# Kernel optimization log

Hardware: AMD Instinct MI355X
Metric: run time of the kernel (lower is better)

The kernel has to match this reference:

```python
import jax, jax.numpy as jnp
import numpy as np

N_NODES = 20000
DEG = 6
E = N_NODES * DEG  # 120000 edges == line-graph nodes
D_NODE, D_EDGE = 64, 16
HID, OUT = 128, 128
EPS = 1e-5


def setup_inputs() -> dict:
    key = jax.random.key(0)
    ks = jax.random.split(key, 8)
    rng = np.random.default_rng(0)
    # graph: each node is the source of DEG edges (direction='out' -> index_r = edge_index[0])
    src = np.repeat(np.arange(N_NODES), DEG)
    dst = rng.integers(0, N_NODES, E)
    edge_index = np.stack([src, dst]).astype(np.int64)
    # two_step_index: ordered pairs of distinct edges sharing a source node
    # (bipartite 2-hop, self loops removed), then GATConv add_self_loops re-appends (i,i)
    ii, jj = np.meshgrid(np.arange(DEG), np.arange(DEG), indexing='ij')
    off = ~np.eye(DEG, dtype=bool)
    ii, jj = ii[off], jj[off]  # DEG*(DEG-1) within-group pairs
    base = (np.arange(N_NODES) * DEG)[:, None]
    s2 = np.concatenate([(base + ii[None, :]).ravel(), np.arange(E)])
    d2 = np.concatenate([(base + jj[None, :]).ravel(), np.arange(E)])
    index_2step = np.stack([s2, d2]).astype(np.int64)  # [2, 720000]
    d_in = D_NODE + D_EDGE
    return {
        "edge_attr": jax.random.normal(ks[0], (E, D_EDGE), jnp.float32),
        "node_attr": jax.random.normal(ks[1], (N_NODES, D_NODE), jnp.float32),
        "bn0_g": jnp.ones((d_in,), jnp.float32),
        "bn0_b": jnp.zeros((d_in,), jnp.float32),
        "W1": jax.random.normal(ks[2], (d_in, HID), jnp.float32) / np.sqrt(d_in).astype(np.float32),
        "bn1_g": jnp.ones((HID,), jnp.float32),
        "bn1_b": jnp.zeros((HID,), jnp.float32),
        "Wg": jax.random.normal(ks[3], (HID, OUT), jnp.float32) / np.sqrt(HID).astype(np.float32),
        "att_src": jax.random.normal(ks[4], (OUT,), jnp.float32) * 0.1,
        "att_dst": jax.random.normal(ks[5], (OUT,), jnp.float32) * 0.1,
        "gat_bias": jnp.zeros((OUT,), jnp.float32),
        "bnf_g": jnp.ones((OUT,), jnp.float32),
        "bnf_b": jnp.zeros((OUT,), jnp.float32),
        "edge_index": jnp.asarray(edge_index),
        "index_2step": jnp.asarray(index_2step),
        "num_nodes": N_NODES,
    }


def batch_norm(x, g, b):
    # training-mode BatchNorm1d (biased variance), like the torch module default
    mu = x.mean(0)
    var = x.var(0)
    return (x - mu) * jax.lax.rsqrt(var + EPS) * g + b


def reference(edge_attr, node_attr, bn0_g, bn0_b, W1, bn1_g, bn1_b,
              Wg, att_src, att_dst, gat_bias, bnf_g, bnf_b,
              edge_index, index_2step, num_nodes):
    index_r = edge_index[0]  # [E] source node of each edge (direction='out')
    # h0: per-edge concat of source-node attrs and edge attrs  [E, Dn+De]
    h0 = jnp.concatenate([node_attr[index_r], edge_attr], axis=1)
    # linear encoder: BN -> Linear(no bias) -> BN -> ReLU (dropout p=0)
    h1 = jax.nn.relu(batch_norm(batch_norm(h0, bn0_g, bn0_b) @ W1, bn1_g, bn1_b))
    # --- GATConv (heads=1) on the line graph given by index_2step ---
    E_ = h1.shape[0]
    x = h1 @ Wg                 # [E, OUT]
    a_src = x @ att_src         # [E]
    a_dst = x @ att_dst         # [E]
    s, d = index_2step[0], index_2step[1]
    e = jax.nn.leaky_relu(a_src[s] + a_dst[d], 0.2)          # [E2]
    e = e - jax.ops.segment_max(e, d, num_segments=E_)[d]    # stable edge-softmax
    ex = jnp.exp(e)
    alpha = ex / (jax.ops.segment_sum(ex, d, num_segments=E_)[d] + 1e-16)
    h2 = jax.ops.segment_sum(alpha[:, None] * x[s], d, num_segments=E_) + gat_bias
    # --- global_add_pool keyed by source node id, then final BatchNorm ---
    h3 = jax.ops.segment_sum(h2, index_r, num_segments=num_nodes)  # [N, OUT]
    return batch_norm(h3, bnf_g, bnf_b)
```

## Files before the change

### kernel.cpp

```cpp
#include <hip/hip_runtime.h>

#define N_NODES 20000
#define DEG 6
#define E_EDGES 120000
#define EPS_BN 1e-5f
#define NBLK 2500
#define EB 48
#define NB 8

#define WS_S0SUM 0
#define WS_S0SQ  80
#define WS_BIAS1 160
#define WS_S1SUM 288
#define WS_S1SQ  1312
#define WS_SC1M  2336
#define WS_SH1M  2464
#define WS_FSUM  2592
#define WS_FSQ   2720
#define WS_STATS_FLOATS 2848
#define WS_WT1   2848
#define WS_WGT   8992

typedef float f32x4 __attribute__((ext_vector_type(4)));
typedef short bf16x8 __attribute__((ext_vector_type(8)));

__device__ __forceinline__ unsigned short f2bf(float f) {
  unsigned u = __float_as_uint(f);
  u += 0x7fffu + ((u >> 16) & 1u);
  return (unsigned short)(u >> 16);
}
__device__ __forceinline__ unsigned pack2bf(float a, float b) {
  return (unsigned)f2bf(a) | ((unsigned)f2bf(b) << 16);
}

__global__ __launch_bounds__(256) void k1_bn0_stats(
    const float* __restrict__ node_attr, const float* __restrict__ edge_attr,
    float* __restrict__ ws) {
  __shared__ float red[256];
  const int t = threadIdx.x;
  const int b = blockIdx.x;
  if (b < 128) {
    const int c = t & 63, rl = t >> 6;
    float s = 0.f, q = 0.f;
    for (int row = b * 4 + rl; row < N_NODES; row += 512) {
      float v = node_attr[row * 64 + c];
      s += v; q += v * v;
    }
    red[t] = s;
    __syncthreads();
    if (t < 64) atomicAdd(&ws[WS_S0SUM + t], red[t] + red[t + 64] + red[t + 128] + red[t + 192]);
    __syncthreads();
    red[t] = q;
    __syncthreads();
    if (t < 64) atomicAdd(&ws[WS_S0SQ + t], red[t] + red[t + 64] + red[t + 128] + red[t + 192]);
  } else {
    const int c = t & 15, rl = t >> 4;
    float s = 0.f, q = 0.f;
    for (int row = (b - 128) * 16 + rl; row < E_EDGES; row += 2048) {
      float v = edge_attr[row * 16 + c];
      s += v; q += v * v;
    }
    red[t] = s;
    __syncthreads();
    if (t < 16) {
      float tot = 0.f;
      #pragma unroll
      for (int k = 0; k < 16; ++k) tot += red[t + 16 * k];
      atomicAdd(&ws[WS_S0SUM + 64 + t], tot);
    }
    __syncthreads();
    red[t] = q;
    __syncthreads();
    if (t < 16) {
      float tot = 0.f;
      #pragma unroll
      for (int k = 0; k < 16; ++k) tot += red[t + 16 * k];
      atomicAdd(&ws[WS_S0SQ + 64 + t], tot);
    }
  }
}

__global__ __launch_bounds__(256) void k0_fold(
    const float* __restrict__ W1, const float* __restrict__ Wg,
    const float* __restrict__ bn0_g, const float* __restrict__ bn0_b,
    float* __restrict__ ws) {
  short* wt1 = (short*)(ws + WS_WT1);
  short* wgt = (short*)(ws + WS_WGT);
  const int t0 = blockIdx.x * 256 + threadIdx.x;
  for (int i = t0; i < 128 * 96; i += 32 * 256) {
    int n = i / 96, k = i % 96;
    float v = 0.f;
    if (k < 80) {
      float cnt = (k < 64) ? (float)N_NODES : (float)E_EDGES;
      float mu = ws[WS_S0SUM + k] / cnt;
      float var = ws[WS_S0SQ + k] / cnt - mu * mu;
      v = W1[k * 128 + n] * (bn0_g[k] * rsqrtf(var + EPS_BN));
    }
    wt1[i] = (short)f2bf(v);
  }
  for (int i = t0; i < 128 * 128; i += 32 * 256) {
    int n = i >> 7, k = i & 127;
    wgt[i] = (short)f2bf(Wg[k * 128 + n]);
  }
  if (blockIdx.x == 0 && threadIdx.x < 128) {
    int n = threadIdx.x;
    float s = 0.f;
    for (int k = 0; k < 80; ++k) {
      float cnt = (k < 64) ? (float)N_NODES : (float)E_EDGES;
      float mu = ws[WS_S0SUM + k] / cnt;
      float var = ws[WS_S0SQ + k] / cnt - mu * mu;
      float sc = bn0_g[k] * rsqrtf(var + EPS_BN);
      s += (bn0_b[k] - mu * sc) * W1[k * 128 + n];
    }
    ws[WS_BIAS1 + n] = s;
  }
}

#define STAGE_INPUTS()                                                         \
  if (t < NB * 16) {                                                           \
    int row = t >> 4, c4 = (t & 15) << 2;                                      \
    float4 v = *(const float4*)&node_attr[(size_t)(g * NB + row) * 64 + c4];   \
    *(uint2*)&n0s[row * 72 + c4] = make_uint2(pack2bf(v.x, v.y), pack2bf(v.z, v.w)); \
  }                                                                            \
  if (t < EB * 4) {                                                            \
    int row = t >> 2, c4 = (t & 3) << 2;                                       \
    float4 v = *(const float4*)&edge_attr[(size_t)(g * EB + row) * 16 + c4];   \
    *(uint2*)&e0s[row * 24 + c4] = make_uint2(pack2bf(v.x, v.y), pack2bf(v.z, v.w)); \
  }                                                                            \
  if (t < 8) zpad[t] = 0;

#define GEMM1_CORE(acc1)                                                       \
  _Pragma("unroll")                                                            \
  for (int ks = 0; ks < 3; ++ks) {                                             \
    bf16x8 bb0 = *(const bf16x8*)&wt1[(Nb + lm) * 96 + ks * 32 + lq * 8];      \
    bf16x8 bb1 = *(const bf16x8*)&wt1[(Nb + 16 + lm) * 96 + ks * 32 + lq * 8]; \
    _Pragma("unroll")                                                          \
    for (int mt = 0; mt < 3; ++mt) {                                           \
      const short* ap;                                                         \
      if (ks < 2) ap = &n0s[rowdiv6[mt] * 72 + ks * 32 + lq * 8];              \
      else ap = (lq < 2) ? &e0s[(mt * 16 + lm) * 24 + lq * 8] : zpad;          \
      bf16x8 a = *(const bf16x8*)ap;                                           \
      acc1[mt][0] = __builtin_amdgcn_mfma_f32_16x16x32_bf16(a, bb0, acc1[mt][0], 0, 0, 0); \
      acc1[mt][1] = __builtin_amdgcn_mfma_f32_16x16x32_bf16(a, bb1, acc1[mt][1], 0, 0, 0); \
    }                                                                          \
  }

__global__ __launch_bounds__(256, 6) void k2_bn1_stats(
    const float* __restrict__ node_attr, const float* __restrict__ edge_attr,
    float* __restrict__ ws) {
  __shared__ __align__(16) short n0s[NB * 72];
  __shared__ __align__(16) short e0s[EB * 24];
  __shared__ __align__(16) short zpad[8];
  const int t = threadIdx.x;
  const int g = blockIdx.x;
  const int l = t & 63, wid = t >> 6;
  const int lm = l & 15, lq = l >> 4;
  const int Nb = wid * 32;
  const short* wt1 = (const short*)(ws + WS_WT1);
  int rowdiv6[3];
  #pragma unroll
  for (int mt = 0; mt < 3; ++mt) rowdiv6[mt] = (mt * 16 + lm) / 6;
  float bias1c[2];
  bias1c[0] = ws[WS_BIAS1 + Nb + lm];
  bias1c[1] = ws[WS_BIAS1 + Nb + 16 + lm];
  STAGE_INPUTS();
  __syncthreads();
  f32x4 acc1[3][2] = {};
  GEMM1_CORE(acc1);
  const int set = g & 7;
  #pragma unroll
  for (int nt = 0; nt < 2; ++nt) {
    float s = 0.f, q = 0.f;
    #pragma unroll
    for (int mt = 0; mt < 3; ++mt)
      #pragma unroll
      for (int r = 0; r < 4; ++r) {
        float v = acc1[mt][nt][r] + bias1c[nt];
        s += v; q += v * v;
      }
    s += __shfl_xor(s, 16); s += __shfl_xor(s, 32);
    q += __shfl_xor(q, 16); q += __shfl_xor(q, 32);
    if (l < 16) {
      int col = Nb + nt * 16 + lm;
      atomicAdd(&ws[WS_S1SUM + set * 128 + col], s);
      atomicAdd(&ws[WS_S1SQ + set * 128 + col], q);
    }
  }
}

__global__ __launch_bounds__(128) void k2b_finalize(
    const float* __restrict__ bn1_g, const float* __restrict__ bn1_b,
    float* __restrict__ ws) {
  const int t = threadIdx.x;
  float s = 0.f, q = 0.f;
  #pragma unroll
  for (int st = 0; st < 8; ++st) {
    s += ws[WS_S1SUM + st * 128 + t];
    q += ws[WS_S1SQ + st * 128 + t];
  }
  const float invE = 1.f / (float)E_EDGES;
  float mu = s * invE;
  float var = q * invE - mu * mu;
  float sc1 = bn1_g[t] * rsqrtf(var + EPS_BN);
  float sh1 = bn1_b[t] - mu * sc1;
  ws[WS_SC1M + t] = sc1;
  ws[WS_SH1M + t] = ws[WS_BIAS1 + t] * sc1 + sh1;
}

__global__ __launch_bounds__(256, 6) void k3_fused(
    const float* __restrict__ node_attr, const float* __restrict__ edge_attr,
    const float* __restrict__ att_src, const float* __restrict__ att_dst,
    const float* __restrict__ gat_bias,
    float* __restrict__ out, float* __restrict__ ws) {
  __shared__ __align__(16) short n0s[NB * 72];
  __shared__ __align__(16) short e0s[EB * 24];
  __shared__ __align__(16) short zpad[8];
  __shared__ __align__(16) short h1s[EB * 136];
  __shared__ float asP[4][EB], adP[4][EB];
  __shared__ float asS[EB], adS[EB], wSm[EB];
  __shared__ float h3L[NB * 128];

  const int t = threadIdx.x;
  const int g = blockIdx.x;
  const int l = t & 63, wid = t >> 6;
  const int lm = l & 15, lq = l >> 4;
  const int Nb = wid * 32;
  const short* wt1 = (const short*)(ws + WS_WT1);
  const short* wgt = (const short*)(ws + WS_WGT);
  int rowdiv6[3];
  #pragma unroll
  for (int mt = 0; mt < 3; ++mt) rowdiv6[mt] = (mt * 16 + lm) / 6;
  float sc1c[2], sh1c[2], atS[2], atD[2];
  #pragma unroll
  for (int nt = 0; nt < 2; ++nt) {
    int col = Nb + nt * 16 + lm;
    sc1c[nt] = ws[WS_SC1M + col];
    sh1c[nt] = ws[WS_SH1M + col];
    atS[nt] = att_src[col];
    atD[nt] = att_dst[col];
  }
  *(f32x4*)&h3L[t * 4] = (f32x4){0.f, 0.f, 0.f, 0.f};
  STAGE_INPUTS();
  __syncthreads();
  {
    f32x4 acc1[3][2] = {};
    GEMM1_CORE(acc1);
    #pragma unroll
    for (int mt = 0; mt < 3; ++mt)
      #pragma unroll
      for (int nt = 0; nt < 2; ++nt)
        #pragma unroll
        for (int r = 0; r < 4; ++r) {
          int row = mt * 16 + lq * 4 + r;
          int col = Nb + nt * 16 + lm;
          float v = fmaxf(acc1[mt][nt][r] * sc1c[nt] + sh1c[nt], 0.f);
          h1s[row * 136 + col] = (short)f2bf(v);
        }
  }
  __syncthreads();
  f32x4 acc2[3][2] = {};
  #pragma unroll
  for (int ks = 0; ks < 4; ++ks) {
    bf16x8 bb0 = *(const bf16x8*)&wgt[(Nb + lm) * 128 + ks * 32 + lq * 8];
    bf16x8 bb1 = *(const bf16x8*)&wgt[(Nb + 16 + lm) * 128 + ks * 32 + lq * 8];
    #pragma unroll
    for (int mt = 0; mt < 3; ++mt) {
      bf16x8 a = *(const bf16x8*)&h1s[(mt * 16 + lm) * 136 + ks * 32 + lq * 8];
      acc2[mt][0] = __builtin_amdgcn_mfma_f32_16x16x32_bf16(a, bb0, acc2[mt][0], 0, 0, 0);
      acc2[mt][1] = __builtin_amdgcn_mfma_f32_16x16x32_bf16(a, bb1, acc2[mt][1], 0, 0, 0);
    }
  }
  #pragma unroll
  for (int mt = 0; mt < 3; ++mt)
    #pragma unroll
    for (int r = 0; r < 4; ++r) {
      float ps = acc2[mt][0][r] * atS[0] + acc2[mt][1][r] * atS[1];
      float pd = acc2[mt][0][r] * atD[0] + acc2[mt][1][r] * atD[1];
      #pragma unroll
      for (int off = 1; off < 16; off <<= 1) {
        ps += __shfl_xor(ps, off);
        pd += __shfl_xor(pd, off);
      }
      if (lm == 0) {
        int row = mt * 16 + lq * 4 + r;
        asP[wid][row] = ps;
        adP[wid][row] = pd;
      }
    }
  __syncthreads();
  if (t < EB) {
    asS[t] = asP[0][t] + asP[1][t] + asP[2][t] + asP[3][t];
    adS[t] = adP[0][t] + adP[1][t] + adP[2][t] + adP[3][t];
    int n = t / 6, i = t % 6, nb6 = n * 6;
    float w = 0.f;
    #pragma unroll
    for (int j = 0; j < 6; ++j) {
      float ad = adS[nb6 + j];
      float e[6], m = -1e30f;
      #pragma unroll
      for (int s = 0; s < 6; ++s) {
        float x = asS[nb6 + s] + ad;
        x = (x > 0.f) ? x : 0.2f * x;
        e[s] = x; m = fmaxf(m, x);
      }
      float den = 0.f;
      #pragma unroll
      for (int s = 0; s < 6; ++s) den += __expf(e[s] - m);
      w += __expf(e[i] - m) / (den + 1e-16f);
    }
    wSm[t] = w;
  }
  __syncthreads();
  #pragma unroll
  for (int mt = 0; mt < 3; ++mt)
    #pragma unroll
    for (int r = 0; r < 4; ++r) {
      int row = mt * 16 + lq * 4 + r;
      float w = wSm[row];
      int nl = row / 6;
      #pragma unroll
      for (int nt = 0; nt < 2; ++nt)
        atomicAdd(&h3L[nl * 128 + Nb + nt * 16 + lm], w * acc2[mt][nt][r]);
    }
  __syncthreads();
  {
    int nslot = t >> 5, c4 = (t & 31) << 2;
    f32x4 v = *(f32x4*)&h3L[nslot * 128 + c4];
    const f32x4 gb = *(const f32x4*)&gat_bias[c4];
    v[0] += 6.f * gb[0]; v[1] += 6.f * gb[1];
    v[2] += 6.f * gb[2]; v[3] += 6.f * gb[3];
    *(f32x4*)&out[(size_t)(g * NB + nslot) * 128 + c4] = v;
  }
}

__global__ __launch_bounds__(256) void k4a_stats(
    const float* __restrict__ out, float* __restrict__ ws) {
  __shared__ float red[8][128];
  const int t = threadIdx.x;
  const int c4 = (t & 31) << 2, rl = t >> 5;
  float fs[4] = {0.f, 0.f, 0.f, 0.f}, fq[4] = {0.f, 0.f, 0.f, 0.f};
  for (int r = blockIdx.x * 8 + rl; r < N_NODES; r += 128 * 8) {
    float4 v = *(const float4*)&out[(size_t)r * 128 + c4];
    fs[0] += v.x; fq[0] += v.x * v.x;
    fs[1] += v.y; fq[1] += v.y * v.y;
    fs[2] += v.z; fq[2] += v.z * v.z;
    fs[3] += v.w; fq[3] += v.w * v.w;
  }
  #pragma unroll
  for (int j = 0; j < 4; ++j) red[rl][c4 + j] = fs[j];
  __syncthreads();
  if (t < 128) {
    float s = 0.f;
    #pragma unroll
    for (int k = 0; k < 8; ++k) s += red[k][t];
    atomicAdd(&ws[WS_FSUM + t], s);
  }
  __syncthreads();
  #pragma unroll
  for (int j = 0; j < 4; ++j) red[rl][c4 + j] = fq[j];
  __syncthreads();
  if (t < 128) {
    float s = 0.f;
    #pragma unroll
    for (int k = 0; k < 8; ++k) s += red[k][t];
    atomicAdd(&ws[WS_FSQ + t], s);
  }
}

__global__ __launch_bounds__(256) void k4b_apply(
    float* __restrict__ out, const float* __restrict__ ws,
    const float* __restrict__ bnf_g, const float* __restrict__ bnf_b) {
  int idx4 = blockIdx.x * 256 + threadIdx.x;
  if (idx4 >= N_NODES * 128 / 4) return;
  int c0 = (idx4 & 31) << 2;
  float4 v = ((float4*)out)[idx4];
  float4 fsv = *(const float4*)&ws[WS_FSUM + c0];
  float4 fqv = *(const float4*)&ws[WS_FSQ + c0];
  float4 g4 = *(const float4*)&bnf_g[c0];
  float4 b4 = *(const float4*)&bnf_b[c0];
  const float invN = 1.f / (float)N_NODES;
  float mu, var, sc;
  mu = fsv.x * invN; var = fqv.x * invN - mu * mu; sc = g4.x * rsqrtf(var + EPS_BN);
  v.x = (v.x - mu) * sc + b4.x;
  mu = fsv.y * invN; var = fqv.y * invN - mu * mu; sc = g4.y * rsqrtf(var + EPS_BN);
  v.y = (v.y - mu) * sc + b4.y;
  mu = fsv.z * invN; var = fqv.z * invN - mu * mu; sc = g4.z * rsqrtf(var + EPS_BN);
  v.z = (v.z - mu) * sc + b4.z;
  mu = fsv.w * invN; var = fqv.w * invN - mu * mu; sc = g4.w * rsqrtf(var + EPS_BN);
  v.w = (v.w - mu) * sc + b4.w;
  ((float4*)out)[idx4] = v;
}

extern "C" void kernel_launch(void* const* d_in, const int* in_sizes, int n_in,
                              void* d_out, int out_size, void* d_ws, size_t ws_size,
                              hipStream_t stream) {
  const float* edge_attr = (const float*)d_in[0];
  const float* node_attr = (const float*)d_in[1];
  const float* bn0_g = (const float*)d_in[2];
  const float* bn0_b = (const float*)d_in[3];
  const float* W1    = (const float*)d_in[4];
  const float* bn1_g = (const float*)d_in[5];
  const float* bn1_b = (const float*)d_in[6];
  const float* Wg    = (const float*)d_in[7];
  const float* att_src = (const float*)d_in[8];
  const float* att_dst = (const float*)d_in[9];
  const float* gat_bias = (const float*)d_in[10];
  const float* bnf_g = (const float*)d_in[11];
  const float* bnf_b = (const float*)d_in[12];
  float* ws = (float*)d_ws;
  float* out = (float*)d_out;

  hipMemsetAsync(d_ws, 0, WS_STATS_FLOATS * sizeof(float), stream);
  k1_bn0_stats<<<256, 256, 0, stream>>>(node_attr, edge_attr, ws);
  k0_fold<<<32, 256, 0, stream>>>(W1, Wg, bn0_g, bn0_b, ws);
  k2_bn1_stats<<<NBLK, 256, 0, stream>>>(node_attr, edge_attr, ws);
  k2b_finalize<<<1, 128, 0, stream>>>(bn1_g, bn1_b, ws);
  k3_fused<<<NBLK, 256, 0, stream>>>(node_attr, edge_attr, att_src, att_dst,
                                     gat_bias, out, ws);
  k4a_stats<<<128, 256, 0, stream>>>(out, ws);
  k4b_apply<<<2500, 256, 0, stream>>>(out, ws, bnf_g, bnf_b);
}
```

Measured before the change: 253.9 us.

## Compute BN1 statistics analytically from input Gram matrix instead of full GEMM pass

Replaces the second full pass that recomputed the first GEMM over all edges just to get BatchNorm1 mean and variance. Instead it builds the 80x80 second-moment (Gram) matrix of the concatenated input features, exploiting that each node row is repeated six times, and derives each output column's sum and sum of squares as quadratic forms with the folded weights. This removes a 2500-block MFMA pass, adding a small Gram kernel with many atomics and a tiny finalize kernel. The risks are fp32 cancellation in the variance formula and a mismatch with the bf16 GEMM used later in the fused kernel.

```diff
diff --git a/kernel.cpp b/kernel.cpp
--- a/kernel.cpp
+++ b/kernel.cpp
@@ -11,15 +11,14 @@
 #define WS_S0SUM 0
 #define WS_S0SQ  80
 #define WS_BIAS1 160
-#define WS_S1SUM 288
-#define WS_S1SQ  1312
-#define WS_SC1M  2336
-#define WS_SH1M  2464
-#define WS_FSUM  2592
-#define WS_FSQ   2720
-#define WS_STATS_FLOATS 2848
-#define WS_WT1   2848
-#define WS_WGT   8992
+#define WS_SC1M  288
+#define WS_SH1M  416
+#define WS_FSUM  544
+#define WS_FSQ   672
+#define WS_G0    800
+#define WS_STATS_FLOATS 7200
+#define WS_WT1   7200
+#define WS_WGT   13344
 
 typedef float f32x4 __attribute__((ext_vector_type(4)));
 typedef short bf16x8 __attribute__((ext_vector_type(8)));
@@ -77,6 +76,84 @@
       for (int k = 0; k < 16; ++k) tot += red[t + 16 * k];
       atomicAdd(&ws[WS_S0SQ + 64 + t], tot);
     }
+  }
+}
+
+__global__ __launch_bounds__(256) void kGram(
+    const float* __restrict__ node_attr, const float* __restrict__ edge_attr,
+    float* __restrict__ ws) {
+  const int t = threadIdx.x;
+  const int b = blockIdx.x;
+  float* G0 = ws + WS_G0;
+  if (b < 128) {
+    __shared__ float rows[4][64];
+    const int i = t >> 2, jb = (t & 3) * 16;
+    f32x4 acc[4] = {};
+    for (int r4 = b * 4; r4 < N_NODES; r4 += 512) {
+      __syncthreads();
+      { int rr = t >> 6, cc = t & 63;
+        rows[rr][cc] = node_attr[(size_t)(r4 + rr) * 64 + cc]; }
+      __syncthreads();
+      #pragma unroll
+      for (int kk = 0; kk < 4; ++kk) {
+        float a = rows[kk][i];
+        #pragma unroll
+        for (int q = 0; q < 4; ++q) {
+          f32x4 v = *(f32x4*)&rows[kk][jb + q * 4];
+          acc[q][0] += a * v[0]; acc[q][1] += a * v[1];
+          acc[q][2] += a * v[2]; acc[q][3] += a * v[3];
+        }
+      }
+    }
+    #pragma unroll
+    for (int q = 0; q < 4; ++q)
+      #pragma unroll
+      for (int e = 0; e < 4; ++e)
+        atomicAdd(&G0[i * 80 + jb + q * 4 + e], 6.f * acc[q][e]);
+  } else if (b < 192) {
+    __shared__ float nrow[4][64];
+    __shared__ float es[4][16];
+    const int i = t >> 2, jb = (t & 3) * 4;
+    f32x4 acc = {};
+    for (int n4 = (b - 128) * 4; n4 < N_NODES; n4 += 256) {
+      __syncthreads();
+      { int rr = t >> 6, cc = t & 63;
+        nrow[rr][cc] = node_attr[(size_t)(n4 + rr) * 64 + cc]; }
+      if (t < 64) {
+        int rr = t >> 4, j = t & 15;
+        float s = 0.f;
+        #pragma unroll
+        for (int kk = 0; kk < 6; ++kk)
+          s += edge_attr[(size_t)((n4 + rr) * 6 + kk) * 16 + j];
+        es[rr][j] = s;
+      }
+      __syncthreads();
+      #pragma unroll
+      for (int kk = 0; kk < 4; ++kk) {
+        float a = nrow[kk][i];
+        f32x4 v = *(f32x4*)&es[kk][jb];
+        acc[0] += a * v[0]; acc[1] += a * v[1];
+        acc[2] += a * v[2]; acc[3] += a * v[3];
+      }
+    }
+    #pragma unroll
+    for (int e = 0; e < 4; ++e) {
+      atomicAdd(&G0[i * 80 + 64 + jb + e], acc[e]);
+      atomicAdd(&G0[(64 + jb + e) * 80 + i], acc[e]);
+    }
+  } else {
+    __shared__ float er[64][16];
+    const int i = t >> 4, j = t & 15;
+    float acc = 0.f;
+    for (int e64 = (b - 192) * 64; e64 < E_EDGES; e64 += 64 * 64) {
+      __syncthreads();
+      *(float4*)&er[t >> 2][(t & 3) * 4] =
+          *(const float4*)&edge_attr[(size_t)e64 * 16 + t * 4];
+      __syncthreads();
+      #pragma unroll
+      for (int kk = 0; kk < 64; ++kk) acc += er[kk][i] * er[kk][j];
+    }
+    atomicAdd(&G0[(64 + i) * 80 + 64 + j], acc);
   }
 }
 
@@ -116,6 +193,52 @@
   }
 }
 
+__global__ __launch_bounds__(128) void kFin(
+    const float* __restrict__ W1, const float* __restrict__ bn0_g,
+    const float* __restrict__ bn1_g, const float* __restrict__ bn1_b,
+    float* __restrict__ ws) {
+  __shared__ float G[80][84];
+  __shared__ float sL[80];
+  __shared__ float aL[16][84];
+  const int t = threadIdx.x;
+  if (t < 80) {
+    float cnt = (t < 64) ? (float)N_NODES : (float)E_EDGES;
+    float mu = ws[WS_S0SUM + t] / cnt;
+    float var = ws[WS_S0SQ + t] / cnt - mu * mu;
+    sL[t] = bn0_g[t] * rsqrtf(var + EPS_BN);
+  }
+  for (int i = t; i < 6400; i += 128) G[i / 80][i % 80] = ws[WS_G0 + i];
+  __syncthreads();
+  const int ci = t >> 3, sl = t & 7;
+  const int c = blockIdx.x * 16 + ci;
+  for (int k = sl; k < 80; k += 8) aL[ci][k] = sL[k] * W1[k * 128 + c];
+  __syncthreads();
+  float part = 0.f;
+  for (int k = sl; k < 80; k += 8) {
+    float dot = 0.f;
+    #pragma unroll 8
+    for (int l = 0; l < 80; ++l) dot += G[k][l] * aL[ci][l];
+    part += aL[ci][k] * dot;
+  }
+  part += __shfl_xor(part, 1);
+  part += __shfl_xor(part, 2);
+  part += __shfl_xor(part, 4);
+  if (sl == 0) {
+    float am = 0.f;
+    for (int k = 0; k < 80; ++k) am += aL[ci][k] * ws[WS_S0SUM + k];
+    float bc = ws[WS_BIAS1 + c];
+    const float invE = 1.f / (float)E_EDGES;
+    float sum1 = am + (float)E_EDGES * bc;
+    float sumsq = part + 2.f * bc * am + (float)E_EDGES * bc * bc;
+    float mu = sum1 * invE;
+    float var = sumsq * invE - mu * mu;
+    float sc1 = bn1_g[c] * rsqrtf(var + EPS_BN);
+    float sh1 = bn1_b[c] - mu * sc1;
+    ws[WS_SC1M + c] = sc1;
+    ws[WS_SH1M + c] = bc * sc1 + sh1;
+  }
+}
+
 #define STAGE_INPUTS()                                                         \
   if (t < NB * 16) {                                                           \
     int row = t >> 4, c4 = (t & 15) << 2;                                      \
@@ -144,68 +267,6 @@
       acc1[mt][1] = __builtin_amdgcn_mfma_f32_16x16x32_bf16(a, bb1, acc1[mt][1], 0, 0, 0); \
     }                                                                          \
   }
-
-__global__ __launch_bounds__(256, 6) void k2_bn1_stats(
-    const float* __restrict__ node_attr, const float* __restrict__ edge_attr,
-    float* __restrict__ ws) {
-  __shared__ __align__(16) short n0s[NB * 72];
-  __shared__ __align__(16) short e0s[EB * 24];
-  __shared__ __align__(16) short zpad[8];
-  const int t = threadIdx.x;
-  const int g = blockIdx.x;
-  const int l = t & 63, wid = t >> 6;
-  const int lm = l & 15, lq = l >> 4;
-  const int Nb = wid * 32;
-  const short* wt1 = (const short*)(ws + WS_WT1);
-  int rowdiv6[3];
-  #pragma unroll
-  for (int mt = 0; mt < 3; ++mt) rowdiv6[mt] = (mt * 16 + lm) / 6;
-  float bias1c[2];
-  bias1c[0] = ws[WS_BIAS1 + Nb + lm];
-  bias1c[1] = ws[WS_BIAS1 + Nb + 16 + lm];
-  STAGE_INPUTS();
-  __syncthreads();
-  f32x4 acc1[3][2] = {};
-  GEMM1_CORE(acc1);
-  const int set = g & 7;
-  #pragma unroll
-  for (int nt = 0; nt < 2; ++nt) {
-    float s = 0.f, q = 0.f;
-    #pragma unroll
-    for (int mt = 0; mt < 3; ++mt)
-      #pragma unroll
-      for (int r = 0; r < 4; ++r) {
-        float v = acc1[mt][nt][r] + bias1c[nt];
-        s += v; q += v * v;
-      }
-    s += __shfl_xor(s, 16); s += __shfl_xor(s, 32);
-    q += __shfl_xor(q, 16); q += __shfl_xor(q, 32);
-    if (l < 16) {
-      int col = Nb + nt * 16 + lm;
-      atomicAdd(&ws[WS_S1SUM + set * 128 + col], s);
-      atomicAdd(&ws[WS_S1SQ + set * 128 + col], q);
-    }
-  }
-}
-
-__global__ __launch_bounds__(128) void k2b_finalize(
-    const float* __restrict__ bn1_g, const float* __restrict__ bn1_b,
-    float* __restrict__ ws) {
-  const int t = threadIdx.x;
-  float s = 0.f, q = 0.f;
-  #pragma unroll
-  for (int st = 0; st < 8; ++st) {
-    s += ws[WS_S1SUM + st * 128 + t];
-    q += ws[WS_S1SQ + st * 128 + t];
-  }
-  const float invE = 1.f / (float)E_EDGES;
-  float mu = s * invE;
-  float var = q * invE - mu * mu;
-  float sc1 = bn1_g[t] * rsqrtf(var + EPS_BN);
-  float sh1 = bn1_b[t] - mu * sc1;
-  ws[WS_SC1M + t] = sc1;
-  ws[WS_SH1M + t] = ws[WS_BIAS1 + t] * sc1 + sh1;
-}
 
 __global__ __launch_bounds__(256, 6) void k3_fused(
     const float* __restrict__ node_attr, const float* __restrict__ edge_attr,
@@ -412,9 +473,9 @@
 
   hipMemsetAsync(d_ws, 0, WS_STATS_FLOATS * sizeof(float), stream);
   k1_bn0_stats<<<256, 256, 0, stream>>>(node_attr, edge_attr, ws);
+  kGram<<<256, 256, 0, stream>>>(node_attr, edge_attr, ws);
   k0_fold<<<32, 256, 0, stream>>>(W1, Wg, bn0_g, bn0_b, ws);
-  k2_bn1_stats<<<NBLK, 256, 0, stream>>>(node_attr, edge_attr, ws);
-  k2b_finalize<<<1, 128, 0, stream>>>(bn1_g, bn1_b, ws);
+  kFin<<<8, 128, 0, stream>>>(W1, bn0_g, bn1_g, bn1_b, ws);
   k3_fused<<<NBLK, 256, 0, stream>>>(node_attr, edge_attr, att_src, att_dst,
                                      gat_bias, out, ws);
   k4a_stats<<<128, 256, 0, stream>>>(out, ws);
```

Result: slower. 333.1 us (+31.2%).
